# Kernel tuning notes

Hardware: AMD Instinct MI355X
Metric: run time of the kernel (lower is better)

The kernel has to match this reference:

```python
import jax, jax.numpy as jnp
import numpy as np

N = 1024      # total ROIs packed across the ragged batch
S = 14        # roi_output_size
C = 256       # conv_dim == feature_size
NC = 80       # num_classes
K = 4         # num_convs
DN = ('NHWC', 'HWIO', 'NHWC')


def setup_inputs() -> dict:
    key = jax.random.key(0)
    ks = jax.random.split(key, 5)
    x = jax.random.normal(ks[0], (N, S, S, C), jnp.float32)
    # 4 identical-shape 3x3 convs (C->C), stacked on a leading axis
    Wc = jax.random.normal(ks[1], (K, 3, 3, C, C), jnp.float32) * 0.03
    bc = jnp.zeros((K, C), jnp.float32)
    # 2x2 stride-2 transpose conv (C->C)
    Wt = jax.random.normal(ks[2], (2, 2, C, C), jnp.float32) * 0.03
    bt = jnp.zeros((C,), jnp.float32)
    # 1x1 mask predictor (C->NC), no activation
    Wm = jax.random.normal(ks[3], (1, 1, C, NC), jnp.float32) * 0.03
    bm = jnp.zeros((NC,), jnp.float32)
    return {"x": x, "Wc": Wc, "bc": bc, "Wt": Wt, "bt": bt, "Wm": Wm, "bm": bm}


def reference(x, Wc, bc, Wt, bt, Wm, bm):
    # Packed-batch equivalent of the nested tf.map_fn: conv math is
    # independent per ROI, so one batched conv over all ROIs is identical.
    for i in range(K):  # fixed small layer count
        x = jax.lax.conv_general_dilated(x, Wc[i], (1, 1), 'SAME', dimension_numbers=DN)
        x = jax.nn.relu(x + bc[i])
    # Conv2DTranspose(kernel=2, stride=2, padding='valid'), relu
    x = jax.lax.conv_transpose(x, Wt, (2, 2), 'VALID', dimension_numbers=DN)
    x = jax.nn.relu(x + bt)
    # 1x1 conv, linear activation -> [N, 28, 28, NC]
    x = jax.lax.conv_general_dilated(x, Wm, (1, 1), 'SAME', dimension_numbers=DN) + bm
    return x
```

## Files before the change

### kernel.cpp

```cpp
#include <hip/hip_runtime.h>


typedef _Float16 f16x8 __attribute__((ext_vector_type(8)));
typedef float    f32x4 __attribute__((ext_vector_type(4)));
typedef unsigned short u16;
typedef unsigned int   u32;

__device__ __forceinline__ u16 f2h(float f) {
  union { _Float16 h; u16 u; } c; c.h = (_Float16)f; return c.u;
}

__device__ __forceinline__ void store8(u16* dst, const u16* o) {
  uint4 v;
  v.x = (u32)o[0] | ((u32)o[1] << 16);
  v.y = (u32)o[2] | ((u32)o[3] << 16);
  v.z = (u32)o[4] | ((u32)o[5] << 16);
  v.w = (u32)o[6] | ((u32)o[7] << 16);
  *(uint4*)dst = v;
}

__global__ void prep_weights(const float* __restrict__ Wc, const float* __restrict__ Wt,
                             const float* __restrict__ Wm,
                             u16* __restrict__ WbP, u16* __restrict__ WtP,
                             u16* __restrict__ WmP) {
  int id = blockIdx.x * 256 + threadIdx.x;
  u16 o[8];
  if (id < 294912) {
    int li = id & 63; int rest = id >> 6;
    int ct = rest & 15; rest >>= 4;
    int kc = rest & 7;  rest >>= 3;
    int co  = ct * 16 + (li & 15);
    int ci0 = kc * 32 + (li >> 4) * 8;
#pragma unroll
    for (int j = 0; j < 8; j++) o[j] = f2h(Wc[(rest * 256 + ci0 + j) * 256 + co]);
    store8(&WbP[id * 8], o);
  } else if (id < 327680) {
    int id2 = id - 294912;
    int li = id2 & 63; int rest = id2 >> 6;
    int ct = rest & 15; rest >>= 4;
    int kc = rest & 7;  rest >>= 3;
    int srcq = 3 - rest;
    int co  = ct * 16 + (li & 15);
    int ci0 = kc * 32 + (li >> 4) * 8;
#pragma unroll
    for (int j = 0; j < 8; j++) o[j] = f2h(Wt[(srcq * 256 + ci0 + j) * 256 + co]);
    store8(&WtP[id2 * 8], o);
  } else if (id < 330240) {
    int id3 = id - 327680;
    int li = id3 & 63; int rest = id3 >> 6;
    int kc = rest / 5, nt = rest % 5;
    int nc  = nt * 16 + (li & 15);
    int ci0 = kc * 32 + (li >> 4) * 8;
#pragma unroll
    for (int j = 0; j < 8; j++) o[j] = f2h(Wm[(ci0 + j) * 80 + nc]);
    store8(&WmP[id3 * 8], o);
  }
}

template <bool INF32, int NF>
__global__ __launch_bounds__(256, NF == 2 ? 3 : 2)
void conv_layer(const void* __restrict__ in_, const u16* __restrict__ WbP,
                const float* __restrict__ bc, u16* __restrict__ out, int layer) {
  __shared__ u16 sA[126 * 128 + 128];
  const int ZP = 126 * 128;
  const int tid = threadIdx.x;
  const int w = tid >> 6, lane = tid & 63, q = lane >> 4, r = lane & 15;
  const int CS = 4 / NF;
  const int roi = blockIdx.x / CS, cs = blockIdx.x % CS;
  const int mhalf = blockIdx.y;
  const int mbase = mhalf * 112;
  const int base_px = mhalf ? 98 : 0;
  const int n_px   = mhalf ? 98 : 126;
  const int rot = (roi + mhalf) % 9;
  if (tid < 64) ((u32*)(sA + ZP))[tid] = 0u;

  int py[7], px[7];
#pragma unroll
  for (int mt = 0; mt < 7; mt++) {
    int p = mbase + mt * 16 + r;
    py[mt] = (p < 196) ? (p / 14) : 1000;
    px[mt] = p % 14;
  }
  f32x4 acc[7][NF];
#pragma unroll
  for (int mt = 0; mt < 7; mt++)
#pragma unroll
    for (int nf = 0; nf < NF; nf++) acc[mt][nf] = (f32x4){0.f, 0.f, 0.f, 0.f};

  const float* xrow = (const float*)in_ + ((size_t)roi * 196 + base_px) * 256;
  const u16*   yrow = (const u16*)in_   + ((size_t)roi * 196 + base_px) * 256;

  const int ct0 = cs * (4 * NF) + w * NF;
  const u16* wb = WbP + (size_t)layer * 589824 + ct0 * 512 + lane * 8;

  f16x8 b0[NF], b1[NF];
#pragma unroll
  for (int nf = 0; nf < NF; nf++)
    b0[nf] = *(const f16x8*)&wb[rot * 65536 + nf * 512];

  for (int kh = 0; kh < 2; kh++) {
    if (kh) __syncthreads();
    if (INF32) {
      for (int c = tid; c < n_px * 32; c += 256) {
        int pix = c >> 5, cc = c & 31;
        const float4 v = *(const float4*)&xrow[pix * 256 + kh * 128 + cc * 4];
        ushort4 h; h.x = f2h(v.x); h.y = f2h(v.y); h.z = f2h(v.z); h.w = f2h(v.w);
        int e = pix * 128 + (((cc >> 1) ^ (pix & 15)) << 3) + ((cc & 1) << 2);
        *(ushort4*)&sA[e] = h;
      }
    } else {
      for (int c = tid; c < n_px * 16; c += 256) {
        int pix = c >> 4, ch = c & 15;
        int e = pix * 128 + ((ch ^ (pix & 15)) << 3);
        *(uint4*)&sA[e] = *(const uint4*)&yrow[pix * 256 + kh * 128 + ch * 8];
      }
    }
    __syncthreads();

    for (int t = 0; t < 9; t++) {
      int tap = t + rot; if (tap >= 9) tap -= 9;
      const int dy = tap / 3 - 1, dx = tap % 3 - 1;
      int base_e[7], sw8[7];
#pragma unroll
      for (int mt = 0; mt < 7; mt++) {
        int ny = py[mt] + dy, nx = px[mt] + dx;
        bool v = ((u32)ny < 14u) && ((u32)nx < 14u);
        int pixg = (ny * 14 + nx) - base_px;
        base_e[mt] = v ? pixg * 128 : ZP;
        sw8[mt]    = v ? ((pixg & 15) << 3) : 0;
      }
#pragma unroll
      for (int kk = 0; kk < 4; kk++) {
        int nt = t, nh = kh, nk = kk + 1;
        if (kk == 3) {
          nk = 0; nt = t + 1;
          if (nt == 9) {
            if (kh == 0) { nt = 0; nh = 1; }
            else         { nt = 8; nh = 1; nk = 3; }
          }
        }
        int ntap = nt + rot; if (ntap >= 9) ntap -= 9;
        const u16* wn = wb + (ntap * 8 + nh * 4 + nk) * 8192;
        const int ck8 = kk * 32 + q * 8;
        if ((kk & 1) == 0) {
#pragma unroll
          for (int nf = 0; nf < NF; nf++) b1[nf] = *(const f16x8*)&wn[nf * 512];
#pragma unroll
          for (int mt = 0; mt < 7; mt++) {
            f16x8 a = *(const f16x8*)&sA[base_e[mt] + (ck8 ^ sw8[mt])];
#pragma unroll
            for (int nf = 0; nf < NF; nf++)
              acc[mt][nf] = __builtin_amdgcn_mfma_f32_16x16x32_f16(a, b0[nf], acc[mt][nf], 0, 0, 0);
          }
        } else {
#pragma unroll
          for (int nf = 0; nf < NF; nf++) b0[nf] = *(const f16x8*)&wn[nf * 512];
#pragma unroll
          for (int mt = 0; mt < 7; mt++) {
            f16x8 a = *(const f16x8*)&sA[base_e[mt] + (ck8 ^ sw8[mt])];
#pragma unroll
            for (int nf = 0; nf < NF; nf++)
              acc[mt][nf] = __builtin_amdgcn_mfma_f32_16x16x32_f16(a, b1[nf], acc[mt][nf], 0, 0, 0);
          }
        }
      }
    }
  }

  float bias[NF];
#pragma unroll
  for (int nf = 0; nf < NF; nf++) bias[nf] = bc[layer * 256 + (ct0 + nf) * 16 + r];
#pragma unroll
  for (int mt = 0; mt < 7; mt++) {
#pragma unroll
    for (int jj = 0; jj < 4; jj++) {
      int p = mbase + mt * 16 + q * 4 + jj;
      if (p < 196) {
#pragma unroll
        for (int nf = 0; nf < NF; nf++) {
          float v = acc[mt][nf][jj] + bias[nf];
          v = fmaxf(v, 0.f);
          out[((size_t)roi * 196 + p) * 256 + (ct0 + nf) * 16 + r] = f2h(v);
        }
      }
    }
  }
}

__global__ __launch_bounds__(256, 2)
void tail_fused(const u16* __restrict__ y4, const u16* __restrict__ WtP,
                const u16* __restrict__ WmP, const float* __restrict__ bt,
                const float* __restrict__ bm, float* __restrict__ out) {
  __shared__ u16 sA[112 * 264 + 128];
  const int ZP = 112 * 264;
  const int tid = threadIdx.x;
  const int w = tid >> 6, lane = tid & 63, q = lane >> 4, r = lane & 15;
  const int roi = blockIdx.x, ab = blockIdx.y, mbase = blockIdx.z * 112;
  const int n_px = mbase ? 84 : 112;
  if (tid < 64) ((u32*)(sA + ZP))[tid] = 0u;

  int offs[7];
#pragma unroll
  for (int mt = 0; mt < 7; mt++) {
    int p = mbase + mt * 16 + r;
    offs[mt] = (p < 196) ? (mt * 16 + r) * 136 : ZP;
  }
  f32x4 acc[7][4];
#pragma unroll
  for (int mt = 0; mt < 7; mt++)
#pragma unroll
    for (int nf = 0; nf < 4; nf++) acc[mt][nf] = (f32x4){0.f, 0.f, 0.f, 0.f};

  const u16* wt = WtP + ab * 65536 + (w * 4) * 512 + lane * 8;
  f16x8 b0[4], b1[4];
#pragma unroll
  for (int nf = 0; nf < 4; nf++) b0[nf] = *(const f16x8*)&wt[nf * 512];

  for (int kh = 0; kh < 2; kh++) {
    if (kh) __syncthreads();
    for (int c = tid; c < n_px * 16; c += 256) {
      int pix = c >> 4, c8 = (c & 15) * 8;
      *(uint4*)&sA[pix * 136 + c8] =
          *(const uint4*)&y4[((size_t)roi * 196 + mbase + pix) * 256 + kh * 128 + c8];
    }
    __syncthreads();
#pragma unroll
    for (int kk = 0; kk < 4; kk++) {
      int nc_ = kh * 4 + kk + 1; if (nc_ > 7) nc_ = 7;
      const u16* wn = wt + nc_ * 8192;
      if ((kk & 1) == 0) {
#pragma unroll
        for (int nf = 0; nf < 4; nf++) b1[nf] = *(const f16x8*)&wn[nf * 512];
#pragma unroll
        for (int mt = 0; mt < 7; mt++) {
          f16x8 a = *(const f16x8*)&sA[offs[mt] + kk * 32 + q * 8];
#pragma unroll
          for (int nf = 0; nf < 4; nf++)
            acc[mt][nf] = __builtin_amdgcn_mfma_f32_16x16x32_f16(a, b0[nf], acc[mt][nf], 0, 0, 0);
        }
      } else {
#pragma unroll
        for (int nf = 0; nf < 4; nf++) b0[nf] = *(const f16x8*)&wn[nf * 512];
#pragma unroll
        for (int mt = 0; mt < 7; mt++) {
          f16x8 a = *(const f16x8*)&sA[offs[mt] + kk * 32 + q * 8];
#pragma unroll
          for (int nf = 0; nf < 4; nf++)
            acc[mt][nf] = __builtin_amdgcn_mfma_f32_16x16x32_f16(a, b1[nf], acc[mt][nf], 0, 0, 0);
        }
      }
    }
  }

  __syncthreads();
  float btv[4];
#pragma unroll
  for (int nf = 0; nf < 4; nf++) btv[nf] = bt[(w * 4 + nf) * 16 + r];
#pragma unroll
  for (int mt = 0; mt < 7; mt++) {
#pragma unroll
    for (int jj = 0; jj < 4; jj++) {
      int row = mt * 16 + q * 4 + jj;
#pragma unroll
      for (int nf = 0; nf < 4; nf++) {
        float v = fmaxf(acc[mt][nf][jj] + btv[nf], 0.f);
        sA[row * 264 + (w * 4 + nf) * 16 + r] = f2h(v);
      }
    }
  }
  __syncthreads();

  float bmv[5];
#pragma unroll
  for (int nt = 0; nt < 5; nt++) bmv[nt] = bm[nt * 16 + r];
  const int a_ = ab >> 1, b_ = ab & 1;
  for (int tt = w; tt < 7; tt += 4) {
    f32x4 a2[5];
#pragma unroll
    for (int nt = 0; nt < 5; nt++) a2[nt] = (f32x4){0.f, 0.f, 0.f, 0.f};
#pragma unroll
    for (int kc = 0; kc < 8; kc++) {
      f16x8 af = *(const f16x8*)&sA[(tt * 16 + r) * 264 + kc * 32 + q * 8];
#pragma unroll
      for (int nt = 0; nt < 5; nt++) {
        f16x8 bw = *(const f16x8*)&WmP[((kc * 5 + nt) * 64 + lane) * 8];
        a2[nt] = __builtin_amdgcn_mfma_f32_16x16x32_f16(af, bw, a2[nt], 0, 0, 0);
      }
    }
#pragma unroll
    for (int jj = 0; jj < 4; jj++) {
      int row = tt * 16 + q * 4 + jj;
      int p = mbase + row;
      if (p < 196) {
        int y = p / 14, x = p % 14;
        size_t base = (size_t)roi * 62720 + (2 * y + a_) * 2240 + (2 * x + b_) * 80;
#pragma unroll
        for (int nt = 0; nt < 5; nt++) out[base + nt * 16 + r] = a2[nt][jj] + bmv[nt];
      }
    }
  }
}

extern "C" void kernel_launch(void* const* d_in, const int* in_sizes, int n_in,
                              void* d_out, int out_size, void* d_ws, size_t ws_size,
                              hipStream_t stream) {
  const float* x  = (const float*)d_in[0];
  const float* Wc = (const float*)d_in[1];
  const float* bc = (const float*)d_in[2];
  const float* Wt = (const float*)d_in[3];
  const float* bt = (const float*)d_in[4];
  const float* Wm = (const float*)d_in[5];
  const float* bm = (const float*)d_in[6];
  float* out = (float*)d_out;

  char* ws = (char*)d_ws;
  u16* WbP = (u16*)(ws);
  u16* WtP = (u16*)(ws + 4718592);
  u16* WmP = (u16*)(ws + 5242880);
  u16* yA  = (u16*)(ws + 6291456);
  u16* yB  = (u16*)(ws + 6291456 + 102760448);

  prep_weights<<<1290, 256, 0, stream>>>(Wc, Wt, Wm, WbP, WtP, WmP);

  conv_layer<true , 4><<<dim3(1024, 2), 256, 0, stream>>>(x,  WbP, bc, yA, 0);
  conv_layer<false, 2><<<dim3(2048, 2), 256, 0, stream>>>(yA, WbP, bc, yB, 1);
  conv_layer<false, 2><<<dim3(2048, 2), 256, 0, stream>>>(yB, WbP, bc, yA, 2);
  conv_layer<false, 2><<<dim3(2048, 2), 256, 0, stream>>>(yA, WbP, bc, yB, 3);

  tail_fused<<<dim3(1024, 4, 2), 256, 0, stream>>>(yB, WtP, WmP, bt, bm, out);
}
```

Measured before the change: 1.499 ms.

## Pad LDS rows instead of XOR swizzle, drop weight prefetch, raise occupancy

Replaces the XOR-swizzled LDS layout with a padded row stride of 136 halves, which simplifies the address math. It also removes the double-buffered weight register prefetch, so B fragments are loaded just before use, and adds a min-waves template parameter so launch bounds can ask for 4 blocks per CU. Layer 0 now uses NF=2 with a 2048-block grid, like the other layers. This cuts register pressure to allow higher occupancy, at the cost of exposing global weight-load latency that the prefetch used to hide and of re-reading the input tile more often in layer 0.

```diff
diff --git a/kernel.cpp b/kernel.cpp
--- a/kernel.cpp
+++ b/kernel.cpp
@@ -57,12 +57,12 @@
   }
 }
 
-template <bool INF32, int NF>
-__global__ __launch_bounds__(256, NF == 2 ? 3 : 2)
+template <bool INF32, int NF, int MINW>
+__global__ __launch_bounds__(256, MINW)
 void conv_layer(const void* __restrict__ in_, const u16* __restrict__ WbP,
                 const float* __restrict__ bc, u16* __restrict__ out, int layer) {
-  __shared__ u16 sA[126 * 128 + 128];
-  const int ZP = 126 * 128;
+  __shared__ u16 sA[126 * 136 + 128];
+  const int ZP = 126 * 136;
   const int tid = threadIdx.x;
   const int w = tid >> 6, lane = tid & 63, q = lane >> 4, r = lane & 15;
   const int CS = 4 / NF;
@@ -93,26 +93,20 @@
   const int ct0 = cs * (4 * NF) + w * NF;
   const u16* wb = WbP + (size_t)layer * 589824 + ct0 * 512 + lane * 8;
 
-  f16x8 b0[NF], b1[NF];
-#pragma unroll
-  for (int nf = 0; nf < NF; nf++)
-    b0[nf] = *(const f16x8*)&wb[rot * 65536 + nf * 512];
-
   for (int kh = 0; kh < 2; kh++) {
     if (kh) __syncthreads();
     if (INF32) {
       for (int c = tid; c < n_px * 32; c += 256) {
-        int pix = c >> 5, cc = c & 31;
-        const float4 v = *(const float4*)&xrow[pix * 256 + kh * 128 + cc * 4];
+        int pix = c >> 5, c4 = (c & 31) * 4;
+        const float4 v = *(const float4*)&xrow[pix * 256 + kh * 128 + c4];
         ushort4 h; h.x = f2h(v.x); h.y = f2h(v.y); h.z = f2h(v.z); h.w = f2h(v.w);
-        int e = pix * 128 + (((cc >> 1) ^ (pix & 15)) << 3) + ((cc & 1) << 2);
-        *(ushort4*)&sA[e] = h;
+        *(ushort4*)&sA[pix * 136 + c4] = h;
       }
     } else {
       for (int c = tid; c < n_px * 16; c += 256) {
-        int pix = c >> 4, ch = c & 15;
-        int e = pix * 128 + ((ch ^ (pix & 15)) << 3);
-        *(uint4*)&sA[e] = *(const uint4*)&yrow[pix * 256 + kh * 128 + ch * 8];
+        int pix = c >> 4, c8 = (c & 15) * 8;
+        *(uint4*)&sA[pix * 136 + c8] =
+            *(const uint4*)&yrow[pix * 256 + kh * 128 + c8];
       }
     }
     __syncthreads();
@@ -120,48 +114,26 @@
     for (int t = 0; t < 9; t++) {
       int tap = t + rot; if (tap >= 9) tap -= 9;
       const int dy = tap / 3 - 1, dx = tap % 3 - 1;
-      int base_e[7], sw8[7];
+      int offs[7];
 #pragma unroll
       for (int mt = 0; mt < 7; mt++) {
         int ny = py[mt] + dy, nx = px[mt] + dx;
         bool v = ((u32)ny < 14u) && ((u32)nx < 14u);
-        int pixg = (ny * 14 + nx) - base_px;
-        base_e[mt] = v ? pixg * 128 : ZP;
-        sw8[mt]    = v ? ((pixg & 15) << 3) : 0;
-      }
+        offs[mt] = v ? ((ny * 14 + nx) - base_px) * 136 : ZP;
+      }
+      const u16* wt_ = wb + (tap * 8 + kh * 4) * 8192;
 #pragma unroll
       for (int kk = 0; kk < 4; kk++) {
-        int nt = t, nh = kh, nk = kk + 1;
-        if (kk == 3) {
-          nk = 0; nt = t + 1;
-          if (nt == 9) {
-            if (kh == 0) { nt = 0; nh = 1; }
-            else         { nt = 8; nh = 1; nk = 3; }
-          }
-        }
-        int ntap = nt + rot; if (ntap >= 9) ntap -= 9;
-        const u16* wn = wb + (ntap * 8 + nh * 4 + nk) * 8192;
-        const int ck8 = kk * 32 + q * 8;
-        if ((kk & 1) == 0) {
-#pragma unroll
-          for (int nf = 0; nf < NF; nf++) b1[nf] = *(const f16x8*)&wn[nf * 512];
-#pragma unroll
-          for (int mt = 0; mt < 7; mt++) {
-            f16x8 a = *(const f16x8*)&sA[base_e[mt] + (ck8 ^ sw8[mt])];
-#pragma unroll
-            for (int nf = 0; nf < NF; nf++)
-              acc[mt][nf] = __builtin_amdgcn_mfma_f32_16x16x32_f16(a, b0[nf], acc[mt][nf], 0, 0, 0);
-          }
-        } else {
-#pragma unroll
-          for (int nf = 0; nf < NF; nf++) b0[nf] = *(const f16x8*)&wn[nf * 512];
-#pragma unroll
-          for (int mt = 0; mt < 7; mt++) {
-            f16x8 a = *(const f16x8*)&sA[base_e[mt] + (ck8 ^ sw8[mt])];
-#pragma unroll
-            for (int nf = 0; nf < NF; nf++)
-              acc[mt][nf] = __builtin_amdgcn_mfma_f32_16x16x32_f16(a, b1[nf], acc[mt][nf], 0, 0, 0);
-          }
+        f16x8 b[NF];
+#pragma unroll
+        for (int nf = 0; nf < NF; nf++)
+          b[nf] = *(const f16x8*)&wt_[kk * 8192 + nf * 512];
+#pragma unroll
+        for (int mt = 0; mt < 7; mt++) {
+          f16x8 a = *(const f16x8*)&sA[offs[mt] + kk * 32 + q * 8];
+#pragma unroll
+          for (int nf = 0; nf < NF; nf++)
+            acc[mt][nf] = __builtin_amdgcn_mfma_f32_16x16x32_f16(a, b[nf], acc[mt][nf], 0, 0, 0);
         }
       }
     }
@@ -322,10 +294,10 @@
 
   prep_weights<<<1290, 256, 0, stream>>>(Wc, Wt, Wm, WbP, WtP, WmP);
 
-  conv_layer<true , 4><<<dim3(1024, 2), 256, 0, stream>>>(x,  WbP, bc, yA, 0);
-  conv_layer<false, 2><<<dim3(2048, 2), 256, 0, stream>>>(yA, WbP, bc, yB, 1);
-  conv_layer<false, 2><<<dim3(2048, 2), 256, 0, stream>>>(yB, WbP, bc, yA, 2);
-  conv_layer<false, 2><<<dim3(2048, 2), 256, 0, stream>>>(yA, WbP, bc, yB, 3);
+  conv_layer<true , 2, 3><<<dim3(2048, 2), 256, 0, stream>>>(x,  WbP, bc, yA, 0);
+  conv_layer<false, 2, 4><<<dim3(2048, 2), 256, 0, stream>>>(yA, WbP, bc, yB, 1);
+  conv_layer<false, 2, 4><<<dim3(2048, 2), 256, 0, stream>>>(yB, WbP, bc, yA, 2);
+  conv_layer<false, 2, 4><<<dim3(2048, 2), 256, 0, stream>>>(yA, WbP, bc, yB, 3);
 
   tail_fused<<<dim3(1024, 4, 2), 256, 0, stream>>>(yB, WtP, WmP, bt, bm, out);
 }
```

New measurement: 1.498 ms. About the same (-0.1%).
